# Kernel optimization log

Measured on AMD Instinct MI355X. Metric: run time of the kernel, lower is better.

## Reference

```python
import jax, jax.numpy as jnp
import numpy as np

V, DS, DF, H, NPASS = 32000, 64, 256, 8, 2
B, L, NB = 2, 1024, 512
EPS = 1e-5


def setup_inputs() -> dict:
    ks = jax.random.split(jax.random.key(0), 20)
    def n(k, shape, scale=0.02):
        return (scale * jax.random.normal(k, shape)).astype(jnp.float32)
    return {
        "token_ids": jax.random.randint(ks[0], (B, L), 0, V),
        "tok_mu": n(ks[1], (V, DS)),
        "tok_log_var": n(ks[2], (V, DS)),
        "tok_raw_alpha": n(ks[3], (V, 1), 1.0),
        "tok_features": n(ks[4], (V, DF)),
        "pos_mu": n(ks[5], (L, DS)),
        "qproj_w": n(ks[6], (H * DS, DS)),
        "qproj_b": jnp.zeros((H * DS,), jnp.float32),
        "hproj_w": n(ks[7], (DF, H * DF)),
        "hproj_b": jnp.zeros((DF,), jnp.float32),
        "mu_up_w": n(ks[8], (DS, 2 * DF)),
        "mu_up_b": jnp.zeros((DS,), jnp.float32),
        "agate_w": n(ks[9], (1, 2 * DF)),
        "agate_b": jnp.zeros((1,), jnp.float32),
        "ffn_w": n(ks[10], (DF, 2 * DF)),
        "ffn_b": jnp.zeros((DF,), jnp.float32),
        "ln_g": jnp.ones((DF,), jnp.float32),
        "ln_b": jnp.zeros((DF,), jnp.float32),
        "lm_w": n(ks[11], (V, DF)),
        "lm_b": jnp.zeros((V,), jnp.float32),
        "blob_mu": n(ks[12], (NB, DS)),
        "blob_lv": n(ks[13], (NB, DS)),
        "blob_ra": n(ks[14], (NB,), 1.0),
        "blob_f": n(ks[15], (NB, DF)),
        "bgate_w": n(ks[16], (1, 2 * DF)),
        "bgate_b": jnp.zeros((1,), jnp.float32),
    }


def _composite_weights(a):
    # front-to-back alpha compositing along last axis: w_j = a_j * prod_{k<j}(1-a_k)
    T = jnp.cumprod(1.0 - a, axis=-1)
    T_ex = jnp.concatenate([jnp.ones_like(T[..., :1]), T[..., :-1]], axis=-1)
    return a * T_ex, T[..., -1]


def _forward(token_ids, tok_mu, tok_log_var, tok_raw_alpha, tok_features, pos_mu,
             qproj_w, qproj_b, hproj_w, hproj_b, mu_up_w, mu_up_b, agate_w, agate_b,
             ffn_w, ffn_b, ln_g, ln_b, lm_w, lm_b, blob_mu, blob_lv, blob_ra, blob_f,
             bgate_w, bgate_b):
    Bc, Lc = token_ids.shape
    mu = tok_mu[token_ids] + pos_mu[:Lc][None]          # [B,L,DS]
    log_var = tok_log_var[token_ids]                     # [B,L,DS]
    alpha = jax.nn.sigmoid(tok_raw_alpha[token_ids][..., 0])  # [B,L]
    features = tok_features[token_ids]                   # [B,L,DF]

    # ---- blob query + blob render ----
    query = mu.mean(axis=1)                              # [B,DS]
    iv_b = jnp.exp(-blob_lv)                             # [NB,DS]
    d2b = (jnp.einsum('bd,nd->bn', query * query, iv_b)
           - 2.0 * jnp.einsum('bd,nd->bn', query, blob_mu * iv_b)
           + jnp.sum(blob_mu * blob_mu * iv_b, -1)[None])
    Kb = jnp.exp(-0.5 * d2b)                             # [B,NB]
    ab = jax.nn.sigmoid(blob_ra)[None] * Kb              # effective alpha
    wb, t_residual = _composite_weights(ab)
    blob_meaning = jnp.einsum('bn,nf->bf', wb, blob_f)   # [B,DF] (blob_proj = Identity)

    # ---- word meaning: multi-pass Gaussian causal render ----
    mask = jnp.tril(jnp.ones((Lc, Lc), jnp.float32))
    iv = jnp.exp(-log_var)                               # inv-variance, fixed across passes
    cur_mu, cur_alpha, cur_feat = mu, alpha, features
    meaning = None
    for p in range(NPASS):
        q = (cur_mu @ qproj_w.T + qproj_b).reshape(Bc, Lc, H, DS).transpose(0, 2, 1, 3)  # [B,H,L,DS]
        # squared Mahalanobis distance via three GEMM-style contractions (no [B,H,L,L,DS] tensor)
        d2 = (jnp.einsum('bhid,bjd->bhij', q * q, iv)
              - 2.0 * jnp.einsum('bhid,bjd->bhij', q, cur_mu * iv)
              + jnp.sum(cur_mu * cur_mu * iv, -1)[:, None, None, :])
        K = jnp.exp(-0.5 * d2)                           # [B,H,L,L]
        a = cur_alpha[:, None, None, :] * K * mask
        w, _ = _composite_weights(a)
        m = jnp.einsum('bhij,bjf->bhif', w, cur_feat)    # [B,H,L,DF]
        m_cat = m.transpose(0, 2, 1, 3).reshape(Bc, Lc, H * DF)
        meaning = m_cat @ hproj_w.T + hproj_b            # [B,L,DF] (dropout = eval/identity)
        if p < NPASS - 1:
            ctx = jnp.concatenate([cur_feat, meaning], axis=-1)  # [B,L,2DF]
            cur_mu = cur_mu + ctx @ mu_up_w.T + mu_up_b
            cur_alpha = cur_alpha * jax.nn.sigmoid(ctx @ agate_w.T + agate_b)[..., 0]
            cur_feat = cur_feat + ctx @ ffn_w.T + ffn_b

    # ---- blob gate fusion ----
    blob_exp = jnp.broadcast_to(blob_meaning[:, None, :], meaning.shape)
    gate = jax.nn.sigmoid(jnp.concatenate([blob_exp, meaning], -1) @ bgate_w.T + bgate_b)  # [B,L,1]
    t_res = t_residual[:, None, None]
    fused = (1.0 - t_res) * gate * blob_exp + t_res * meaning

    # ---- final layernorm + lm head ----
    mean = fused.mean(-1, keepdims=True)
    var = ((fused - mean) ** 2).mean(-1, keepdims=True)
    h = (fused - mean) * jax.lax.rsqrt(var + EPS) * ln_g + ln_b
    logits = h @ lm_w.T + lm_b                           # [B,L,V]
    return logits


def reference(token_ids, tok_mu, tok_log_var, tok_raw_alpha, tok_features, pos_mu,
              qproj_w, qproj_b, hproj_w, hproj_b, mu_up_w, mu_up_b, agate_w, agate_b,
              ffn_w, ffn_b, ln_g, ln_b, lm_w, lm_b, blob_mu, blob_lv, blob_ra, blob_f,
              bgate_w, bgate_b):
    return _forward(token_ids, tok_mu, tok_log_var, tok_raw_alpha, tok_features, pos_mu,
                    qproj_w, qproj_b, hproj_w, hproj_b, mu_up_w, mu_up_b, agate_w, agate_b,
                    ffn_w, ffn_b, ln_g, ln_b, lm_w, lm_b, blob_mu, blob_lv, blob_ra, blob_f,
                    bgate_w, bgate_b)
```

## Files before the change

kernel.cpp:

```cpp
#include <hip/hip_runtime.h>
#include <hip/hip_bf16.h>
#include <cstdint>
#include <cstddef>

#define V_   32000
#define DS_  64
#define DF_  256
#define H_   8
#define L_   1024
#define B_   2
#define NB_  512
#define BL_  2048
#define EPS_ 1e-5f

typedef unsigned short ushort_t;
typedef unsigned int uint_t;
typedef short bf16x8 __attribute__((ext_vector_type(8)));
typedef float f32x4 __attribute__((ext_vector_type(4)));
#define AS1 __attribute__((address_space(1)))
#define AS3 __attribute__((address_space(3)))

__device__ __forceinline__ float sigmoidf_(float x) { return 1.f / (1.f + __expf(-x)); }
__device__ __forceinline__ ushort_t f2bf(float x) {
    __hip_bfloat16 b = __float2bfloat16(x);
    return __builtin_bit_cast(ushort_t, b);
}
__device__ __forceinline__ uint_t packbf(float lo, float hi) {
    return ((uint_t)f2bf(hi) << 16) | (uint_t)f2bf(lo);
}
__device__ __forceinline__ float bflo(uint_t v) {
    return __builtin_bit_cast(float, v << 16);
}
__device__ __forceinline__ float bfhi(uint_t v) {
    return __builtin_bit_cast(float, v & 0xFFFF0000u);
}

__device__ __forceinline__ float block_reduce_sum(float v, float* red) {
    int t = threadIdx.x;
    red[t] = v;
    __syncthreads();
    for (int s = 128; s > 0; s >>= 1) {
        if (t < s) red[t] += red[t + s];
        __syncthreads();
    }
    float r = red[0];
    __syncthreads();
    return r;
}

__global__ __launch_bounds__(256) void k_cvt5(
    const float* __restrict__ s0, ushort_t* __restrict__ d0,
    const float* __restrict__ s1, ushort_t* __restrict__ d1,
    const float* __restrict__ s2, ushort_t* __restrict__ d2,
    const float* __restrict__ s3, ushort_t* __restrict__ d3,
    const float* __restrict__ s4, ushort_t* __restrict__ d4) {
    int blk = blockIdx.x;
    const float* s; ushort_t* d; int base;
    if (blk < 32)        { s = s0; d = d0; base = blk; }
    else if (blk < 64)   { s = s1; d = d1; base = blk - 32; }
    else if (blk < 192)  { s = s2; d = d2; base = blk - 64; }
    else if (blk < 704)  { s = s3; d = d3; base = blk - 192; }
    else                 { s = s4; d = d4; base = blk - 704; }
    int i = (base * 256 + threadIdx.x) * 4;
    float4 v = *reinterpret_cast<const float4*>(s + i);
    ushort4 o = {f2bf(v.x), f2bf(v.y), f2bf(v.z), f2bf(v.w)};
    *reinterpret_cast<ushort4*>(d + i) = o;
}

__global__ __launch_bounds__(256) void k_gather(
    const int* __restrict__ tok, const float* __restrict__ tok_mu,
    const float* __restrict__ tok_lv, const float* __restrict__ tok_ra,
    const float* __restrict__ tok_f, const float* __restrict__ pos_mu,
    float* __restrict__ mu, ushort_t* __restrict__ mub16,
    uint_t* __restrict__ muivP, float* __restrict__ alpha,
    float* __restrict__ feat, ushort_t* __restrict__ featb16,
    ushort_t* __restrict__ fTg) {
    int row = blockIdx.x;
    int b = row >> 10;
    int l = row & (L_ - 1);
    int t = threadIdx.x;
    int v = tok[row];
    if (t < DS_) {
        float m = tok_mu[(size_t)v * DS_ + t] + pos_mu[l * DS_ + t];
        mu[(size_t)row * DS_ + t] = m;
        mub16[(size_t)row * DS_ + t] = f2bf(m);
        float ivv = __expf(-tok_lv[(size_t)v * DS_ + t]);
        muivP[(size_t)t * BL_ + row] = packbf(m, ivv);
    }
    float fv = tok_f[(size_t)v * DF_ + t];
    feat[(size_t)row * DF_ + t] = fv;
    featb16[(size_t)row * DF_ + t] = f2bf(fv);
    {
        int jb = (l >> 3) & 7, jr = l & 7;
        int jp = (l & ~63) | ((jb ^ (t & 7)) << 3) | jr;
        fTg[((size_t)(b * DF_ + t) << 10) + jp] = f2bf(fv);
    }
    if (t == 0) alpha[row] = sigmoidf_(tok_ra[v]);
}

__global__ __launch_bounds__(256) void k_queryblob(
    const float* __restrict__ mu, const float* __restrict__ blob_mu,
    const float* __restrict__ blob_lv, const float* __restrict__ blob_ra,
    const float* __restrict__ blob_f, float* __restrict__ blobm,
    float* __restrict__ tres) {
    __shared__ float red[256];
    __shared__ float sq[DS_];
    __shared__ float sa[NB_];
    __shared__ float sp[NB_];
    int b = blockIdx.x, t = threadIdx.x;
    int d = t & 63, c = t >> 6;
    float s = 0.f;
    for (int l = c; l < L_; l += 4) s += mu[((size_t)b * L_ + l) * DS_ + d];
    red[t] = s;
    __syncthreads();
    if (c == 0)
        sq[d] = (red[d] + red[64 + d] + red[128 + d] + red[192 + d]) * (1.f / L_);
    __syncthreads();
    for (int n = t; n < NB_; n += 256) {
        float d2 = 0.f;
        for (int dd = 0; dd < DS_; ++dd) {
            float diff = sq[dd] - blob_mu[n * DS_ + dd];
            d2 += __expf(-blob_lv[n * DS_ + dd]) * diff * diff;
        }
        float a = sigmoidf_(blob_ra[n]) * __expf(-0.5f * d2);
        sa[n] = a;
        sp[n] = 1.f - a;
    }
    __syncthreads();
    int n0 = t, n1 = t + 256;
    for (int s2 = 1; s2 < NB_; s2 <<= 1) {
        float t0 = (n0 >= s2) ? sp[n0 - s2] : 1.f;
        float t1 = (n1 >= s2) ? sp[n1 - s2] : 1.f;
        __syncthreads();
        sp[n0] *= t0;
        sp[n1] *= t1;
        __syncthreads();
    }
    float w0 = sa[n0] * (n0 ? sp[n0 - 1] : 1.f);
    float w1 = sa[n1] * sp[n1 - 1];
    __syncthreads();
    sa[n0] = w0;
    sa[n1] = w1;
    if (t == 0) tres[b] = sp[NB_ - 1];
    __syncthreads();
    float acc = 0.f;
    for (int n = 0; n < NB_; ++n) acc += sa[n] * blob_f[n * DF_ + t];
    blobm[b * DF_ + t] = acc;
}

__global__ __launch_bounds__(512) void k_attn5(
    const float* __restrict__ q, const uint_t* __restrict__ muivP,
    const float* __restrict__ alpha, const ushort_t* __restrict__ fTg,
    ushort_t* __restrict__ mcatb) {
    __shared__ __align__(16) uint_t smiu[64 * 64];
    __shared__ __align__(16) ushort_t sfT[256 * 64];
    __shared__ __align__(16) ushort_t sw16[16][72];
    __shared__ float sq[H_][64];
    __shared__ float sT[H_];
    int tid = threadIdx.x;
    int w = tid >> 6, lane = tid & 63;
    int bid = blockIdx.x;
    int b = bid >> 10, i = bid & (L_ - 1);
    int row = b * L_ + i;
    const int lr = lane & 15, q4 = lane >> 4;

    for (int k = tid; k < 16 * 72; k += 512) ((ushort_t*)sw16)[k] = 0;
    sq[w][lane] = q[(size_t)row * 512 + tid];

    float T = 1.f;
    f32x4 acc0 = {}, acc1 = {};

    for (int j0 = 0; j0 <= i; j0 += 64) {
        __syncthreads();
        if (j0 > 0) {
            bool alive = false;
            #pragma unroll
            for (int h = 0; h < H_; ++h) alive |= (sT[h] >= 1e-12f);
            if (!alive) break;
        }
        {
            const uint_t* src = muivP + b * L_ + j0;
            #pragma unroll
            for (int r = 0; r < 2; ++r) {
                int d = w * 8 + r * 4 + q4;
                const uint_t* gp = src + (size_t)d * BL_ + lr * 4;
                __builtin_amdgcn_global_load_lds((const AS1 uint_t*)gp,
                    (AS3 uint_t*)&smiu[(w * 8 + r * 4) * 64], 16, 0, 0);
            }
        }
        {
            #pragma unroll
            for (int it = 0; it < 4; ++it) {
                int c0 = w * 32 + it * 8;
                const ushort_t* gp = fTg +
                    ((size_t)(b * DF_ + c0 + (lane >> 3)) << 10) + j0 + (lane & 7) * 8;
                __builtin_amdgcn_global_load_lds((const AS1 uint_t*)gp,
                    (AS3 uint_t*)&sfT[c0 * 64], 16, 0, 0);
            }
        }
        __syncthreads();

        int jj = j0 + lane;
        float d2a = 0.f;
        #pragma unroll 8
        for (int d = 0; d < 64; ++d) {
            uint_t v = smiu[d * 64 + lane];
            float m = bflo(v), iv = bfhi(v);
            float diff = sq[w][d] - m;
            d2a = fmaf(iv * diff, diff, d2a);
        }
        float a = (jj <= i) ? alpha[b * L_ + jj] * __expf(-0.5f * d2a) : 0.f;

        float p = 1.f - a;
        #pragma unroll
        for (int s = 1; s < 64; s <<= 1) {
            float tt = __shfl_up(p, s, 64);
            if (lane >= s) p *= tt;
        }
        float Tex = __shfl_up(p, 1, 64);
        if (lane == 0) Tex = 1.f;
        sw16[w][lane] = f2bf(a * T * Tex);
        float Tch = __shfl(p, 63, 64);
        T *= Tch;
        if (lane == 0) sT[w] = T;
        __syncthreads();

        #pragma unroll
        for (int kk = 0; kk < 2; ++kk) {
            bf16x8 afr = *reinterpret_cast<const bf16x8*>(
                (const char*)sw16 + lr * 144 + kk * 64 + q4 * 16);
            {
                int c = (w * 2 + 0) * 16 + lr;
                int bo = c * 128 + ((kk * 64 + q4 * 16) ^ ((c & 7) << 4));
                bf16x8 bfr = *reinterpret_cast<const bf16x8*>((const char*)sfT + bo);
                acc0 = __builtin_amdgcn_mfma_f32_16x16x32_bf16(afr, bfr, acc0, 0, 0, 0);
            }
            {
                int c = (w * 2 + 1) * 16 + lr;
                int bo = c * 128 + ((kk * 64 + q4 * 16) ^ ((c & 7) << 4));
                bf16x8 bfr = *reinterpret_cast<const bf16x8*>((const char*)sfT + bo);
                acc1 = __builtin_amdgcn_mfma_f32_16x16x32_bf16(afr, bfr, acc1, 0, 0, 0);
            }
        }
    }
    if (q4 < 2) {
        #pragma unroll
        for (int r = 0; r < 4; ++r) {
            int h = q4 * 4 + r;
            int c0 = (w * 2 + 0) * 16 + lr;
            int c1 = (w * 2 + 1) * 16 + lr;
            mcatb[(size_t)row * 2048 + h * 256 + c0] = f2bf(acc0[r]);
            mcatb[(size_t)row * 2048 + h * 256 + c1] = f2bf(acc1[r]);
        }
    }
}

template <int BM, int BN, int BK, int WGM, int WGN, bool NTS, bool WB16>
__global__ __launch_bounds__(256) void gemm_mfma2(
    const ushort_t* __restrict__ A, const ushort_t* __restrict__ A2, int K1,
    int strideA, const ushort_t* __restrict__ W, const float* __restrict__ bias,
    float* __restrict__ C, ushort_t* __restrict__ Cb, int M, int N, int K) {
    constexpr int WMF = BM / WGM / 16;
    constexpr int WNF = BN / WGN / 16;
    constexpr int KK  = BK / 32;
    constexpr int AHALF = BM * BK;
// ... 53 lines not shown
        for (int mi = 0; mi < WMF; ++mi)
            #pragma unroll
            for (int kk = 0; kk < KK; ++kk)
                af[mi][kk] = *reinterpret_cast<const bf16x8*>(
                    &Ab[((kk * 4 + q4) * BM + wr * (BM / WGM) + mi * 16 + lr) * 8]);
        #pragma unroll
        for (int ni = 0; ni < WNF; ++ni)
            #pragma unroll
            for (int kk = 0; kk < KK; ++kk)
                bfr[ni][kk] = *reinterpret_cast<const bf16x8*>(
                    &Bb[((kk * 4 + q4) * BN + wc * (BN / WGN) + ni * 16 + lr) * 8]);
        #pragma unroll
        for (int kk = 0; kk < KK; ++kk)
            #pragma unroll
            for (int mi = 0; mi < WMF; ++mi)
                #pragma unroll
                for (int ni = 0; ni < WNF; ++ni)
                    acc[mi][ni] = __builtin_amdgcn_mfma_f32_16x16x32_bf16(
                        af[mi][kk], bfr[ni][kk], acc[mi][ni], 0, 0, 0);
        __syncthreads();
    }

    float* tile = (float*)smem;
    #pragma unroll
    for (int mi = 0; mi < WMF; ++mi)
        #pragma unroll
        for (int ni = 0; ni < WNF; ++ni) {
            int col = wc * (BN / WGN) + ni * 16 + lr;
            float bv = bias[n0 + col];
            #pragma unroll
            for (int j = 0; j < 4; ++j) {
                int r2 = wr * (BM / WGM) + mi * 16 + q4 * 4 + j;
                tile[r2 * BN + col] = acc[mi][ni][j] + bv;
            }
        }
    __syncthreads();
    constexpr int EV = (BM * BN / 4) / 256;
    #pragma unroll
    for (int e = 0; e < EV; ++e) {
        int idx = e * 256 + tid;
        int r = idx / (BN / 4), c4 = idx % (BN / 4);
        f32x4 v = reinterpret_cast<const f32x4*>(tile)[idx];
        f32x4* dst = reinterpret_cast<f32x4*>(&C[(size_t)(m0 + r) * N + n0 + c4 * 4]);
        if (NTS) __builtin_nontemporal_store(v, dst);
        else *dst = v;
        if (WB16) {
            ushort4 ob = {f2bf(v[0]), f2bf(v[1]), f2bf(v[2]), f2bf(v[3])};
            *reinterpret_cast<ushort4*>(&Cb[(size_t)(m0 + r) * N + n0 + c4 * 4]) = ob;
        }
    }
}

__global__ __launch_bounds__(256) void k_apply(
    const float* __restrict__ meaning, const float* __restrict__ agw,
    const float* __restrict__ agb, const float* __restrict__ dmu,
    const float* __restrict__ dffn, float* __restrict__ mu,
    ushort_t* __restrict__ mub16, uint_t* __restrict__ muivP,
    float* __restrict__ alpha, float* __restrict__ feat,
    ushort_t* __restrict__ featb16, ushort_t* __restrict__ fTg) {
    __shared__ float red[256];
    int row = blockIdx.x, t = threadIdx.x;
    int b = row >> 10;
    int l = row & (L_ - 1);
    float c0 = feat[(size_t)row * DF_ + t];
    float c1 = meaning[(size_t)row * DF_ + t];
    float s = block_reduce_sum(c0 * agw[t] + c1 * agw[256 + t], red);
    if (t == 0) alpha[row] *= sigmoidf_(s + agb[0]);
    if (t < DS_) {
        float m = mu[(size_t)row * DS_ + t] + dmu[(size_t)row * DS_ + t];
        mu[(size_t)row * DS_ + t] = m;
        mub16[(size_t)row * DS_ + t] = f2bf(m);
        uint_t v = muivP[(size_t)t * BL_ + row];
        muivP[(size_t)t * BL_ + row] = (v & 0xFFFF0000u) | (uint_t)f2bf(m);
    }
    float fn = c0 + dffn[(size_t)row * DF_ + t];
    feat[(size_t)row * DF_ + t] = fn;
    featb16[(size_t)row * DF_ + t] = f2bf(fn);
    {
        int jb = (l >> 3) & 7, jr = l & 7;
        int jp = (l & ~63) | ((jb ^ (t & 7)) << 3) | jr;
        fTg[((size_t)(b * DF_ + t) << 10) + jp] = f2bf(fn);
    }
}

__global__ __launch_bounds__(256) void k_fused_ln(
    const float* __restrict__ meaning, const float* __restrict__ blobm,
    const float* __restrict__ tres, const float* __restrict__ bgw,
    const float* __restrict__ bgb, const float* __restrict__ ln_g,
    const float* __restrict__ ln_b, ushort_t* __restrict__ houtb) {
    __shared__ float red[256];
    int row = blockIdx.x, t = threadIdx.x;
    int b = row >> 10;
    float m = meaning[(size_t)row * DF_ + t];
    float be = blobm[b * DF_ + t];
    float tr = tres[b];
    float gsum = block_reduce_sum(be * bgw[t] + m * bgw[256 + t], red);
    float gate = sigmoidf_(gsum + bgb[0]);
    float f = (1.f - tr) * gate * be + tr * m;
    float mean = block_reduce_sum(f, red) * (1.f / DF_);
    float d = f - mean;
    float var = block_reduce_sum(d * d, red) * (1.f / DF_);
    houtb[(size_t)row * DF_ + t] = f2bf(d * rsqrtf(var + EPS_) * ln_g[t] + ln_b[t]);
}

extern "C" void kernel_launch(void* const* d_in, const int* in_sizes, int n_in,
                              void* d_out, int out_size, void* d_ws, size_t ws_size,
                              hipStream_t stream) {
    const int*   tok      = (const int*)d_in[0];
    const float* tok_mu   = (const float*)d_in[1];
    const float* tok_lv   = (const float*)d_in[2];
    const float* tok_ra   = (const float*)d_in[3];
    const float* tok_f    = (const float*)d_in[4];
    const float* pos_mu   = (const float*)d_in[5];
    const float* qproj_w  = (const float*)d_in[6];
    const float* qproj_b  = (const float*)d_in[7];
    const float* hproj_w  = (const float*)d_in[8];
    const float* hproj_b  = (const float*)d_in[9];
    const float* mu_up_w  = (const float*)d_in[10];
    const float* mu_up_b  = (const float*)d_in[11];
    const float* agate_w  = (const float*)d_in[12];
    const float* agate_b  = (const float*)d_in[13];
    const float* ffn_w    = (const float*)d_in[14];
    const float* ffn_b    = (const float*)d_in[15];
    const float* ln_g     = (const float*)d_in[16];
    const float* ln_b     = (const float*)d_in[17];
    const float* lm_w     = (const float*)d_in[18];
    const float* lm_b     = (const float*)d_in[19];
    const float* blob_mu  = (const float*)d_in[20];
    const float* blob_lv  = (const float*)d_in[21];
    const float* blob_ra  = (const float*)d_in[22];
    const float* blob_f   = (const float*)d_in[23];
    const float* bgate_w  = (const float*)d_in[24];
    const float* bgate_b  = (const float*)d_in[25];
    float* out = (float*)d_out;

    float* ws = (float*)d_ws;
    float* mu      = ws;
    float* alpha   = mu + BL_ * DS_;
    float* feat    = alpha + BL_;
    float* blobm   = feat + BL_ * DF_;
    float* tres    = blobm + B_ * DF_;
    float* q       = tres + 64;
    float* meaning = q + BL_ * 512;
    float* dmu     = meaning + BL_ * DF_;
    float* dffn    = dmu + BL_ * DS_;
    uint_t* muivP  = (uint_t*)(dffn + BL_ * DF_);
    ushort_t* fTg   = (ushort_t*)(muivP + (size_t)DS_ * BL_);
    ushort_t* mub16 = fTg + (size_t)B_ * DF_ * L_;
    ushort_t* featb16 = mub16 + (size_t)BL_ * DS_;
    ushort_t* meanb16 = featb16 + (size_t)BL_ * DF_;
    ushort_t* mcatb = meanb16 + (size_t)BL_ * DF_;
    ushort_t* hbufb = mcatb + (size_t)BL_ * 2048;
    ushort_t* wbf   = hbufb + (size_t)BL_ * DF_;
    ushort_t* hpwbf = wbf + (size_t)V_ * DF_;
    ushort_t* qpwbf = hpwbf + (size_t)DF_ * 2048;
    ushort_t* muwbf = qpwbf + (size_t)512 * 64;
    ushort_t* ffnwbf = muwbf + (size_t)64 * 512;

    k_cvt5<<<8704, 256, 0, stream>>>(qproj_w, qpwbf, mu_up_w, muwbf,
                                     ffn_w, ffnwbf, hproj_w, hpwbf, lm_w, wbf);

    k_gather<<<BL_, 256, 0, stream>>>(tok, tok_mu, tok_lv, tok_ra, tok_f, pos_mu,
                                      mu, mub16, muivP, alpha, feat, featb16, fTg);
    k_queryblob<<<B_, 256, 0, stream>>>(mu, blob_mu, blob_lv, blob_ra, blob_f,
                                        blobm, tres);

    for (int p = 0; p < 2; ++p) {
        gemm_mfma2<32, 32, 64, 2, 2, false, false>
            <<<dim3(BL_ / 32, 512 / 32), 256, 0, stream>>>(
            mub16, nullptr, 0, DS_, qpwbf, qproj_b, q, nullptr, BL_, 512, DS_);
        k_attn5<<<BL_, 512, 0, stream>>>(q, muivP, alpha, fTg, mcatb);
        if (p == 0) {
            gemm_mfma2<32, 32, 64, 2, 2, false, true>
                <<<dim3(BL_ / 32, DF_ / 32), 256, 0, stream>>>(
                mcatb, nullptr, 0, H_ * DF_, hpwbf, hproj_b, meaning, meanb16,
                BL_, DF_, H_ * DF_);
            gemm_mfma2<32, 32, 64, 2, 2, false, false>
                <<<dim3(BL_ / 32, DS_ / 32), 256, 0, stream>>>(
                featb16, meanb16, DF_, DF_, muwbf, mu_up_b, dmu, nullptr,
                BL_, DS_, 512);
            gemm_mfma2<32, 32, 64, 2, 2, false, false>
                <<<dim3(BL_ / 32, DF_ / 32), 256, 0, stream>>>(
                featb16, meanb16, DF_, DF_, ffnwbf, ffn_b, dffn, nullptr,
                BL_, DF_, 512);
            k_apply<<<BL_, 256, 0, stream>>>(meaning, agate_w, agate_b, dmu, dffn,
                                             mu, mub16, muivP, alpha, feat,
                                             featb16, fTg);
        } else {
            gemm_mfma2<32, 32, 64, 2, 2, false, false>
                <<<dim3(BL_ / 32, DF_ / 32), 256, 0, stream>>>(
                mcatb, nullptr, 0, H_ * DF_, hpwbf, hproj_b, meaning, nullptr,
                BL_, DF_, H_ * DF_);
        }
    }

    k_fused_ln<<<BL_, 256, 0, stream>>>(meaning, blobm, tres, bgate_w, bgate_b,
                                        ln_g, ln_b, hbufb);
    gemm_mfma2<128, 128, 64, 2, 2, true, false>
        <<<dim3(BL_ / 128, V_ / 128), 256, 0, stream>>>(
        hbufb, nullptr, 0, DF_, wbf, lm_b, out, nullptr, BL_, V_, DF_);
}
```

Measured before the change: 314.9 us.

## Expand Mahalanobis distance into MFMA dot products and merge setup kernels

The per-key scalar loop over 64 dims in the attention kernel is replaced by an algebraic expansion, sum(iv*q^2) - 2*sum(iv*m*q) + sum(m^2*iv). The first two terms become a 16x16x32 bf16 MFMA between per-head [q^2, -2q] rows and per-key [iv, m*iv] rows stored in a swizzled row layout. The constant term is folded into a precomputed alphaC. The conversion, gather and query-blob kernels are merged into one launch, and the blob query now recomputes mu from tokens itself. The expansion adds cancellation error in bf16, and the distance is used inside exp.

```diff
diff --git a/kernel.cpp b/kernel.cpp
--- a/kernel.cpp
+++ b/kernel.cpp
@@ -25,14 +25,8 @@
     __hip_bfloat16 b = __float2bfloat16(x);
     return __builtin_bit_cast(ushort_t, b);
 }
-__device__ __forceinline__ uint_t packbf(float lo, float hi) {
-    return ((uint_t)f2bf(hi) << 16) | (uint_t)f2bf(lo);
-}
-__device__ __forceinline__ float bflo(uint_t v) {
-    return __builtin_bit_cast(float, v << 16);
-}
-__device__ __forceinline__ float bfhi(uint_t v) {
-    return __builtin_bit_cast(float, v & 0xFFFF0000u);
+__device__ __forceinline__ float bf2f(ushort_t u) {
+    return __builtin_bit_cast(float, (uint_t)u << 16);
 }
 
 __device__ __forceinline__ float block_reduce_sum(float v, float* red) {
@@ -48,114 +42,130 @@
     return r;
 }
 
-__global__ __launch_bounds__(256) void k_cvt5(
-    const float* __restrict__ s0, ushort_t* __restrict__ d0,
-    const float* __restrict__ s1, ushort_t* __restrict__ d1,
-    const float* __restrict__ s2, ushort_t* __restrict__ d2,
-    const float* __restrict__ s3, ushort_t* __restrict__ d3,
-    const float* __restrict__ s4, ushort_t* __restrict__ d4) {
-    int blk = blockIdx.x;
-    const float* s; ushort_t* d; int base;
-    if (blk < 32)        { s = s0; d = d0; base = blk; }
-    else if (blk < 64)   { s = s1; d = d1; base = blk - 32; }
-    else if (blk < 192)  { s = s2; d = d2; base = blk - 64; }
-    else if (blk < 704)  { s = s3; d = d3; base = blk - 192; }
-    else                 { s = s4; d = d4; base = blk - 704; }
-    int i = (base * 256 + threadIdx.x) * 4;
-    float4 v = *reinterpret_cast<const float4*>(s + i);
-    ushort4 o = {f2bf(v.x), f2bf(v.y), f2bf(v.z), f2bf(v.w)};
-    *reinterpret_cast<ushort4*>(d + i) = o;
-}
-
-__global__ __launch_bounds__(256) void k_gather(
+#define NCVT_ 8704
+#define NGA_  (NCVT_ + BL_)
+#define NST_  (NGA_ + B_)
+__global__ __launch_bounds__(256) void k_setup(
     const int* __restrict__ tok, const float* __restrict__ tok_mu,
     const float* __restrict__ tok_lv, const float* __restrict__ tok_ra,
     const float* __restrict__ tok_f, const float* __restrict__ pos_mu,
+    const float* __restrict__ qproj_w, const float* __restrict__ mu_up_w,
+    const float* __restrict__ ffn_w, const float* __restrict__ hproj_w,
+    const float* __restrict__ lm_w, const float* __restrict__ blob_mu,
+    const float* __restrict__ blob_lv, const float* __restrict__ blob_ra,
+    const float* __restrict__ blob_f,
+    ushort_t* __restrict__ qpwbf, ushort_t* __restrict__ muwbf,
+    ushort_t* __restrict__ ffnwbf, ushort_t* __restrict__ hpwbf,
+    ushort_t* __restrict__ wbf,
     float* __restrict__ mu, ushort_t* __restrict__ mub16,
-    uint_t* __restrict__ muivP, float* __restrict__ alpha,
-    float* __restrict__ feat, ushort_t* __restrict__ featb16,
-    ushort_t* __restrict__ fTg) {
-    int row = blockIdx.x;
-    int b = row >> 10;
-    int l = row & (L_ - 1);
+    ushort_t* __restrict__ qkb, float* __restrict__ alpha,
+    float* __restrict__ alphaC, float* __restrict__ feat,
+    ushort_t* __restrict__ featb16, ushort_t* __restrict__ fTg,
+    float* __restrict__ blobm, float* __restrict__ tres) {
+    int blk = blockIdx.x;
     int t = threadIdx.x;
-    int v = tok[row];
-    if (t < DS_) {
-        float m = tok_mu[(size_t)v * DS_ + t] + pos_mu[l * DS_ + t];
-        mu[(size_t)row * DS_ + t] = m;
-        mub16[(size_t)row * DS_ + t] = f2bf(m);
-        float ivv = __expf(-tok_lv[(size_t)v * DS_ + t]);
-        muivP[(size_t)t * BL_ + row] = packbf(m, ivv);
-    }
-    float fv = tok_f[(size_t)v * DF_ + t];
-    feat[(size_t)row * DF_ + t] = fv;
-    featb16[(size_t)row * DF_ + t] = f2bf(fv);
-    {
+    if (blk < NCVT_) {
+        const float* s; ushort_t* d; int base;
+        if (blk < 32)        { s = qproj_w; d = qpwbf;  base = blk; }
+        else if (blk < 64)   { s = mu_up_w; d = muwbf;  base = blk - 32; }
+        else if (blk < 192)  { s = ffn_w;   d = ffnwbf; base = blk - 64; }
+        else if (blk < 704)  { s = hproj_w; d = hpwbf;  base = blk - 192; }
+        else                 { s = lm_w;    d = wbf;    base = blk - 704; }
+        int i = (base * 256 + t) * 4;
+        float4 v = *reinterpret_cast<const float4*>(s + i);
+        ushort4 o = {f2bf(v.x), f2bf(v.y), f2bf(v.z), f2bf(v.w)};
+        *reinterpret_cast<ushort4*>(d + i) = o;
+        return;
+    }
+    if (blk < NGA_) {
+        int row = blk - NCVT_;
+        int l = row & (L_ - 1);
+        int v = tok[row];
+        if (t < DS_) {
+            float m = tok_mu[(size_t)v * DS_ + t] + pos_mu[l * DS_ + t];
+            mu[(size_t)row * DS_ + t] = m;
+            mub16[(size_t)row * DS_ + t] = f2bf(m);
+            float ivv = __expf(-tok_lv[(size_t)v * DS_ + t]);
+            int sw = (row & 7) << 3;
+            qkb[(size_t)row * 128 + (t ^ sw)] = f2bf(ivv);
+            qkb[(size_t)row * 128 + 64 + (t ^ sw)] = f2bf(m * ivv);
+            float term = m * m * ivv;
+            #pragma unroll
+            for (int s2 = 1; s2 < 64; s2 <<= 1) term += __shfl_xor(term, s2, 64);
+            if (t == 0) {
+                float al = sigmoidf_(tok_ra[v]);
+                alpha[row] = al;
+                alphaC[row] = al * __expf(-0.5f * term);
+            }
+        }
+        float fv = tok_f[(size_t)v * DF_ + t];
+        feat[(size_t)row * DF_ + t] = fv;
+        featb16[(size_t)row * DF_ + t] = f2bf(fv);
         int jb = (l >> 3) & 7, jr = l & 7;
         int jp = (l & ~63) | ((jb ^ (t & 7)) << 3) | jr;
-        fTg[((size_t)(b * DF_ + t) << 10) + jp] = f2bf(fv);
-    }
-    if (t == 0) alpha[row] = sigmoidf_(tok_ra[v]);
-}
-
-__global__ __launch_bounds__(256) void k_queryblob(
-    const float* __restrict__ mu, const float* __restrict__ blob_mu,
-    const float* __restrict__ blob_lv, const float* __restrict__ blob_ra,
-    const float* __restrict__ blob_f, float* __restrict__ blobm,
-    float* __restrict__ tres) {
-    __shared__ float red[256];
-    __shared__ float sq[DS_];
-    __shared__ float sa[NB_];
-    __shared__ float sp[NB_];
-    int b = blockIdx.x, t = threadIdx.x;
-    int d = t & 63, c = t >> 6;
-    float s = 0.f;
-    for (int l = c; l < L_; l += 4) s += mu[((size_t)b * L_ + l) * DS_ + d];
-    red[t] = s;
-    __syncthreads();
-    if (c == 0)
-        sq[d] = (red[d] + red[64 + d] + red[128 + d] + red[192 + d]) * (1.f / L_);
-    __syncthreads();
-    for (int n = t; n < NB_; n += 256) {
-        float d2 = 0.f;
-        for (int dd = 0; dd < DS_; ++dd) {
-            float diff = sq[dd] - blob_mu[n * DS_ + dd];
-            d2 += __expf(-blob_lv[n * DS_ + dd]) * diff * diff;
-        }
-        float a = sigmoidf_(blob_ra[n]) * __expf(-0.5f * d2);
-        sa[n] = a;
-        sp[n] = 1.f - a;
-    }
-    __syncthreads();
-    int n0 = t, n1 = t + 256;
-    for (int s2 = 1; s2 < NB_; s2 <<= 1) {
-        float t0 = (n0 >= s2) ? sp[n0 - s2] : 1.f;
-        float t1 = (n1 >= s2) ? sp[n1 - s2] : 1.f;
-        __syncthreads();
-        sp[n0] *= t0;
-        sp[n1] *= t1;
-        __syncthreads();
-    }
-    float w0 = sa[n0] * (n0 ? sp[n0 - 1] : 1.f);
-    float w1 = sa[n1] * sp[n1 - 1];
-    __syncthreads();
-    sa[n0] = w0;
-    sa[n1] = w1;
-    if (t == 0) tres[b] = sp[NB_ - 1];
-    __syncthreads();
-    float acc = 0.f;
-    for (int n = 0; n < NB_; ++n) acc += sa[n] * blob_f[n * DF_ + t];
-    blobm[b * DF_ + t] = acc;
-}
-
-__global__ __launch_bounds__(512) void k_attn5(
-    const float* __restrict__ q, const uint_t* __restrict__ muivP,
-    const float* __restrict__ alpha, const ushort_t* __restrict__ fTg,
+        fTg[((size_t)((row >> 10) * DF_ + t) << 10) + jp] = f2bf(fv);
+        return;
+    }
+    {
+        __shared__ float red[256];
+        __shared__ int stok[L_];
+        __shared__ float sq[DS_];
+        __shared__ float sa[NB_];
+        __shared__ float sp[NB_];
+        int b = blk - NGA_;
+        for (int l = t; l < L_; l += 256) stok[l] = tok[b * L_ + l];
+        __syncthreads();
+        int d = t & 63, c = t >> 6;
+        float s = 0.f;
+        for (int l = c; l < L_; l += 4)
+            s += tok_mu[(size_t)stok[l] * DS_ + d] + pos_mu[l * DS_ + d];
+        red[t] = s;
+        __syncthreads();
+        if (c == 0)
+            sq[d] = (red[d] + red[64 + d] + red[128 + d] + red[192 + d]) * (1.f / L_);
+        __syncthreads();
+        for (int n = t; n < NB_; n += 256) {
+            float d2 = 0.f;
+            for (int dd = 0; dd < DS_; ++dd) {
+                float diff = sq[dd] - blob_mu[n * DS_ + dd];
+                d2 += __expf(-blob_lv[n * DS_ + dd]) * diff * diff;
+            }
+            float a = sigmoidf_(blob_ra[n]) * __expf(-0.5f * d2);
+            sa[n] = a;
+            sp[n] = 1.f - a;
+        }
+        __syncthreads();
+        int n0 = t, n1 = t + 256;
+        for (int s2 = 1; s2 < NB_; s2 <<= 1) {
+            float t0 = (n0 >= s2) ? sp[n0 - s2] : 1.f;
+            float t1 = (n1 >= s2) ? sp[n1 - s2] : 1.f;
+            __syncthreads();
+            sp[n0] *= t0;
+            sp[n1] *= t1;
+            __syncthreads();
+        }
+        float w0 = sa[n0] * (n0 ? sp[n0 - 1] : 1.f);
+        float w1 = sa[n1] * sp[n1 - 1];
+        __syncthreads();
+        sa[n0] = w0;
+        sa[n1] = w1;
+        if (t == 0) tres[b] = sp[NB_ - 1];
+        __syncthreads();
+        float acc = 0.f;
+        for (int n = 0; n < NB_; ++n) acc += sa[n] * blob_f[n * DF_ + t];
+        blobm[b * DF_ + t] = acc;
+    }
+}
+
+__global__ __launch_bounds__(512) void k_attn6(
+    const float* __restrict__ q, const ushort_t* __restrict__ qkb,
+    const float* __restrict__ alphaC, const ushort_t* __restrict__ fTg,
     ushort_t* __restrict__ mcatb) {
-    __shared__ __align__(16) uint_t smiu[64 * 64];
+    __shared__ __align__(16) ushort_t sQK[64 * 128];
     __shared__ __align__(16) ushort_t sfT[256 * 64];
+    __shared__ __align__(16) ushort_t sA[16 * 128];
     __shared__ __align__(16) ushort_t sw16[16][72];
-    __shared__ float sq[H_][64];
+    __shared__ float sE[H_][64];
     __shared__ float sT[H_];
     int tid = threadIdx.x;
     int w = tid >> 6, lane = tid & 63;
@@ -164,8 +174,14 @@
     int row = b * L_ + i;
     const int lr = lane & 15, q4 = lane >> 4;
 
-    for (int k = tid; k < 16 * 72; k += 512) ((ushort_t*)sw16)[k] = 0;
-    sq[w][lane] = q[(size_t)row * 512 + tid];
+    for (int k = tid; k < 8 * 128; k += 512) sA[8 * 128 + k] = 0;
+    for (int k = tid; k < 8 * 72; k += 512) ((ushort_t*)sw16)[8 * 72 + k] = 0;
+    {
+        float qv = q[(size_t)row * 512 + tid];
+        int sw = (w & 7) << 3;
+        sA[w * 128 + (lane ^ sw)] = f2bf(qv * qv);
+        sA[w * 128 + 64 + (lane ^ sw)] = f2bf(-2.f * qv);
+    }
 
     float T = 1.f;
     f32x4 acc0 = {}, acc1 = {};
@@ -179,13 +195,13 @@
             if (!alive) break;
         }
         {
-            const uint_t* src = muivP + b * L_ + j0;
-            #pragma unroll
-            for (int r = 0; r < 2; ++r) {
-                int d = w * 8 + r * 4 + q4;
-                const uint_t* gp = src + (size_t)d * BL_ + lr * 4;
-                __builtin_amdgcn_global_load_lds((const AS1 uint_t*)gp,
-                    (AS3 uint_t*)&smiu[(w * 8 + r * 4) * 64], 16, 0, 0);
+            const ushort_t* src = qkb + (size_t)(b * L_ + j0) * 128;
+            #pragma unroll
+            for (int it = 0; it < 2; ++it) {
+                int c = it * 512 + w * 64;
+                __builtin_amdgcn_global_load_lds(
+                    (const AS1 uint_t*)(src + (size_t)(c + lane) * 8),
+                    (AS3 uint_t*)&sQK[c * 8], 16, 0, 0);
             }
         }
         {
@@ -200,17 +216,28 @@
         }
         __syncthreads();
 
-        int jj = j0 + lane;
-        float d2a = 0.f;
-        #pragma unroll 8
-        for (int d = 0; d < 64; ++d) {
-            uint_t v = smiu[d * 64 + lane];
-            float m = bflo(v), iv = bfhi(v);
-            float diff = sq[w][d] - m;
-            d2a = fmaf(iv * diff, diff, d2a);
-        }
-        float a = (jj <= i) ? alpha[b * L_ + jj] * __expf(-0.5f * d2a) : 0.f;
-
+        if (w < 4) {
+            int jj = j0 + w * 16 + lr;
+            float alc = (jj <= i) ? alphaC[b * L_ + jj] : 0.f;
+            f32x4 dacc = {};
+            int j = w * 16 + lr;
+            int swj = (j & 7) << 3;
+            int swa = (lr & 7) << 3;
+            #pragma unroll
+            for (int ks = 0; ks < 4; ++ks) {
+                bf16x8 afr = *reinterpret_cast<const bf16x8*>(
+                    &sA[lr * 128 + ((ks * 32 + q4 * 8) ^ swa)]);
+                bf16x8 bfr = *reinterpret_cast<const bf16x8*>(
+                    &sQK[j * 128 + ((ks * 32 + q4 * 8) ^ swj)]);
+                dacc = __builtin_amdgcn_mfma_f32_16x16x32_bf16(afr, bfr, dacc, 0, 0, 0);
+            }
+            #pragma unroll
+            for (int r = 0; r < 4; ++r)
+                sE[q4 * 4 + r][w * 16 + lr] = alc * __expf(-0.5f * dacc[r]);
+        }
+        __syncthreads();
+
+        float a = sE[w][lane];
         float p = 1.f - a;
         #pragma unroll
         for (int s = 1; s < 64; s <<= 1) {
@@ -373,23 +400,32 @@
     const float* __restrict__ meaning, const float* __restrict__ agw,
     const float* __restrict__ agb, const float* __restrict__ dmu,
     const float* __restrict__ dffn, float* __restrict__ mu,
-    ushort_t* __restrict__ mub16, uint_t* __restrict__ muivP,
-    float* __restrict__ alpha, float* __restrict__ feat,
-    ushort_t* __restrict__ featb16, ushort_t* __restrict__ fTg) {
+    ushort_t* __restrict__ mub16, ushort_t* __restrict__ qkb,
+    float* __restrict__ alpha, float* __restrict__ alphaC,
+    float* __restrict__ feat, ushort_t* __restrict__ featb16,
+    ushort_t* __restrict__ fTg) {
     __shared__ float red[256];
     int row = blockIdx.x, t = threadIdx.x;
-    int b = row >> 10;
     int l = row & (L_ - 1);
     float c0 = feat[(size_t)row * DF_ + t];
     float c1 = meaning[(size_t)row * DF_ + t];
     float s = block_reduce_sum(c0 * agw[t] + c1 * agw[256 + t], red);
-    if (t == 0) alpha[row] *= sigmoidf_(s + agb[0]);
+    float gate = sigmoidf_(s + agb[0]);
     if (t < DS_) {
         float m = mu[(size_t)row * DS_ + t] + dmu[(size_t)row * DS_ + t];
         mu[(size_t)row * DS_ + t] = m;
         mub16[(size_t)row * DS_ + t] = f2bf(m);
-        uint_t v = muivP[(size_t)t * BL_ + row];
-        muivP[(size_t)t * BL_ + row] = (v & 0xFFFF0000u) | (uint_t)f2bf(m);
+        int sw = (row & 7) << 3;
+        float ivv = bf2f(qkb[(size_t)row * 128 + (t ^ sw)]);
+        qkb[(size_t)row * 128 + 64 + (t ^ sw)] = f2bf(m * ivv);
+        float term = m * m * ivv;
+        #pragma unroll
+        for (int s2 = 1; s2 < 64; s2 <<= 1) term += __shfl_xor(term, s2, 64);
+        if (t == 0) {
+            float aN = alpha[row] * gate;
+            alpha[row] = aN;
+            alphaC[row] = aN * __expf(-0.5f * term);
+        }
     }
     float fn = c0 + dffn[(size_t)row * DF_ + t];
     feat[(size_t)row * DF_ + t] = fn;
@@ -397,7 +433,7 @@
     {
         int jb = (l >> 3) & 7, jr = l & 7;
         int jp = (l & ~63) | ((jb ^ (t & 7)) << 3) | jr;
-        fTg[((size_t)(b * DF_ + t) << 10) + jp] = f2bf(fn);
+        fTg[((size_t)((row >> 10) * DF_ + t) << 10) + jp] = f2bf(fn);
     }
 }
 
@@ -455,15 +491,16 @@
     float* ws = (float*)d_ws;
     float* mu      = ws;
     float* alpha   = mu + BL_ * DS_;
-    float* feat    = alpha + BL_;
+    float* alphaC  = alpha + BL_;
+    float* feat    = alphaC + BL_;
     float* blobm   = feat + BL_ * DF_;
     float* tres    = blobm + B_ * DF_;
     float* q       = tres + 64;
     float* meaning = q + BL_ * 512;
     float* dmu     = meaning + BL_ * DF_;
     float* dffn    = dmu + BL_ * DS_;
-    uint_t* muivP  = (uint_t*)(dffn + BL_ * DF_);
-    ushort_t* fTg   = (ushort_t*)(muivP + (size_t)DS_ * BL_);
+    ushort_t* qkb   = (ushort_t*)(dffn + BL_ * DF_);
+    ushort_t* fTg   = qkb + (size_t)BL_ * 128;
     ushort_t* mub16 = fTg + (size_t)B_ * DF_ * L_;
     ushort_t* featb16 = mub16 + (size_t)BL_ * DS_;
     ushort_t* meanb16 = featb16 + (size_t)BL_ * DF_;
@@ -475,19 +512,18 @@
     ushort_t* muwbf = qpwbf + (size_t)512 * 64;
     ushort_t* ffnwbf = muwbf + (size_t)64 * 512;
 
-    k_cvt5<<<8704, 256, 0, stream>>>(qproj_w, qpwbf, mu_up_w, muwbf,
-                                     ffn_w, ffnwbf, hproj_w, hpwbf, lm_w, wbf);
-
-    k_gather<<<BL_, 256, 0, stream>>>(tok, tok_mu, tok_lv, tok_ra, tok_f, pos_mu,
-                                      mu, mub16, muivP, alpha, feat, featb16, fTg);
-    k_queryblob<<<B_, 256, 0, stream>>>(mu, blob_mu, blob_lv, blob_ra, blob_f,
-                                        blobm, tres);
+    k_setup<<<NST_, 256, 0, stream>>>(
+        tok, tok_mu, tok_lv, tok_ra, tok_f, pos_mu,
+        qproj_w, mu_up_w, ffn_w, hproj_w, lm_w,
+        blob_mu, blob_lv, blob_ra, blob_f,
+        qpwbf, muwbf, ffnwbf, hpwbf, wbf,
+        mu, mub16, qkb, alpha, alphaC, feat, featb16, fTg, blobm, tres);
 
     for (int p = 0; p < 2; ++p) {
         gemm_mfma2<32, 32, 64, 2, 2, false, false>
             <<<dim3(BL_ / 32, 512 / 32), 256, 0, stream>>>(
             mub16, nullptr, 0, DS_, qpwbf, qproj_b, q, nullptr, BL_, 512, DS_);
-        k_attn5<<<BL_, 512, 0, stream>>>(q, muivP, alpha, fTg, mcatb);
+        k_attn6<<<BL_, 512, 0, stream>>>(q, qkb, alphaC, fTg, mcatb);
         if (p == 0) {
             gemm_mfma2<32, 32, 64, 2, 2, false, true>
                 <<<dim3(BL_ / 32, DF_ / 32), 256, 0, stream>>>(
@@ -502,8 +538,8 @@
                 featb16, meanb16, DF_, DF_, ffnwbf, ffn_b, dffn, nullptr,
                 BL_, DF_, 512);
             k_apply<<<BL_, 256, 0, stream>>>(meaning, agate_w, agate_b, dmu, dffn,
-                                             mu, mub16, muivP, alpha, feat,
-                                             featb16, fTg);
+                                             mu, mub16, qkb, alpha, alphaC,
+                                             feat, featb16, fTg);
         } else {
             gemm_mfma2<32, 32, 64, 2, 2, false, false>
                 <<<dim3(BL_ / 32, DF_ / 32), 256, 0, stream>>>(
```

New measurement: 319.6 us. About the same (+1.5%).

## Merge setup kernels and fuse mu_up/ffn/agate GEMMs into one concatenated GEMM

Applied to the files above, without the earlier changes.

Combines the weight conversion, token gather and blob-query kernels into one launch. The blob query now recomputes the mean of mu directly from the token tables, so it no longer depends on the gather output. The mu_up, ffn and alpha-gate projections are stacked into one 352-column weight matrix, so a single GEMM replaces two GEMMs plus a block reduction in k_apply. The K tile for the h-projection and fused GEMMs also goes from 64 to 128. This cuts launch count and redundant reads, but the gate dot product is now done in bf16 and the setup kernel is less uniform.

```diff
diff --git a/kernel.cpp b/kernel.cpp
--- a/kernel.cpp
+++ b/kernel.cpp
@@ -48,104 +48,139 @@
     return r;
 }
 
-__global__ __launch_bounds__(256) void k_cvt5(
-    const float* __restrict__ s0, ushort_t* __restrict__ d0,
-    const float* __restrict__ s1, ushort_t* __restrict__ d1,
-    const float* __restrict__ s2, ushort_t* __restrict__ d2,
-    const float* __restrict__ s3, ushort_t* __restrict__ d3,
-    const float* __restrict__ s4, ushort_t* __restrict__ d4) {
-    int blk = blockIdx.x;
-    const float* s; ushort_t* d; int base;
-    if (blk < 32)        { s = s0; d = d0; base = blk; }
-    else if (blk < 64)   { s = s1; d = d1; base = blk - 32; }
-    else if (blk < 192)  { s = s2; d = d2; base = blk - 64; }
-    else if (blk < 704)  { s = s3; d = d3; base = blk - 192; }
-    else                 { s = s4; d = d4; base = blk - 704; }
-    int i = (base * 256 + threadIdx.x) * 4;
-    float4 v = *reinterpret_cast<const float4*>(s + i);
-    ushort4 o = {f2bf(v.x), f2bf(v.y), f2bf(v.z), f2bf(v.w)};
-    *reinterpret_cast<ushort4*>(d + i) = o;
-}
-
-__global__ __launch_bounds__(256) void k_gather(
+#define NCVT_ 8720
+#define NGA_  (NCVT_ + BL_)
+#define NST_  (NGA_ + B_)
+__global__ __launch_bounds__(256) void k_setup(
     const int* __restrict__ tok, const float* __restrict__ tok_mu,
     const float* __restrict__ tok_lv, const float* __restrict__ tok_ra,
     const float* __restrict__ tok_f, const float* __restrict__ pos_mu,
+    const float* __restrict__ qproj_w, const float* __restrict__ mu_up_w,
+    const float* __restrict__ mu_up_b, const float* __restrict__ ffn_w,
+    const float* __restrict__ ffn_b, const float* __restrict__ agate_w,
+    const float* __restrict__ agate_b, const float* __restrict__ hproj_w,
+    const float* __restrict__ lm_w, const float* __restrict__ blob_mu,
+    const float* __restrict__ blob_lv, const float* __restrict__ blob_ra,
+    const float* __restrict__ blob_f,
+    ushort_t* __restrict__ qpwbf, ushort_t* __restrict__ cwbf,
+    ushort_t* __restrict__ hpwbf, ushort_t* __restrict__ wbf,
+    float* __restrict__ cbias,
     float* __restrict__ mu, ushort_t* __restrict__ mub16,
     uint_t* __restrict__ muivP, float* __restrict__ alpha,
     float* __restrict__ feat, ushort_t* __restrict__ featb16,
-    ushort_t* __restrict__ fTg) {
-    int row = blockIdx.x;
-    int b = row >> 10;
-    int l = row & (L_ - 1);
+    ushort_t* __restrict__ fTg, float* __restrict__ blobm,
+    float* __restrict__ tres) {
+    int blk = blockIdx.x;
     int t = threadIdx.x;
-    int v = tok[row];
-    if (t < DS_) {
-        float m = tok_mu[(size_t)v * DS_ + t] + pos_mu[l * DS_ + t];
-        mu[(size_t)row * DS_ + t] = m;
-        mub16[(size_t)row * DS_ + t] = f2bf(m);
-        float ivv = __expf(-tok_lv[(size_t)v * DS_ + t]);
-        muivP[(size_t)t * BL_ + row] = packbf(m, ivv);
-    }
-    float fv = tok_f[(size_t)v * DF_ + t];
-    feat[(size_t)row * DF_ + t] = fv;
-    featb16[(size_t)row * DF_ + t] = f2bf(fv);
-    {
+    if (blk < 32) {
+        int i = (blk * 256 + t) * 4;
+        float4 v = *reinterpret_cast<const float4*>(qproj_w + i);
+        ushort4 o = {f2bf(v.x), f2bf(v.y), f2bf(v.z), f2bf(v.w)};
+        *reinterpret_cast<ushort4*>(qpwbf + i) = o;
+        return;
+    }
+    if (blk < 208) {
+        int i = ((blk - 32) * 256 + t) * 4;
+        int r = i >> 9, c = i & 511;
+        float4 v = {0.f, 0.f, 0.f, 0.f};
+        if (r < 64)        v = *reinterpret_cast<const float4*>(mu_up_w + r * 512 + c);
+        else if (r < 320)  v = *reinterpret_cast<const float4*>(ffn_w + (r - 64) * 512 + c);
+        else if (r == 320) v = *reinterpret_cast<const float4*>(agate_w + c);
+        ushort4 o = {f2bf(v.x), f2bf(v.y), f2bf(v.z), f2bf(v.w)};
+        *reinterpret_cast<ushort4*>(cwbf + i) = o;
+        return;
+    }
+    if (blk < 720) {
+        int i = ((blk - 208) * 256 + t) * 4;
+        float4 v = *reinterpret_cast<const float4*>(hproj_w + i);
+        ushort4 o = {f2bf(v.x), f2bf(v.y), f2bf(v.z), f2bf(v.w)};
+        *reinterpret_cast<ushort4*>(hpwbf + i) = o;
+        return;
+    }
+    if (blk < NCVT_) {
+        int i = ((blk - 720) * 256 + t) * 4;
+        float4 v = *reinterpret_cast<const float4*>(lm_w + i);
+        ushort4 o = {f2bf(v.x), f2bf(v.y), f2bf(v.z), f2bf(v.w)};
+        *reinterpret_cast<ushort4*>(wbf + i) = o;
+        return;
+    }
+    if (blk < NGA_) {
+        int row = blk - NCVT_;
+        int l = row & (L_ - 1);
+        int v = tok[row];
+        if (t < DS_) {
+            float m = tok_mu[(size_t)v * DS_ + t] + pos_mu[l * DS_ + t];
+            mu[(size_t)row * DS_ + t] = m;
+            mub16[(size_t)row * DS_ + t] = f2bf(m);
+            float ivv = __expf(-tok_lv[(size_t)v * DS_ + t]);
+            muivP[(size_t)t * BL_ + row] = packbf(m, ivv);
+        }
+        float fv = tok_f[(size_t)v * DF_ + t];
+        feat[(size_t)row * DF_ + t] = fv;
+        featb16[(size_t)row * DF_ + t] = f2bf(fv);
         int jb = (l >> 3) & 7, jr = l & 7;
         int jp = (l & ~63) | ((jb ^ (t & 7)) << 3) | jr;
-        fTg[((size_t)(b * DF_ + t) << 10) + jp] = f2bf(fv);
-    }
-    if (t == 0) alpha[row] = sigmoidf_(tok_ra[v]);
-}
-
-__global__ __launch_bounds__(256) void k_queryblob(
-    const float* __restrict__ mu, const float* __restrict__ blob_mu,
-    const float* __restrict__ blob_lv, const float* __restrict__ blob_ra,
-    const float* __restrict__ blob_f, float* __restrict__ blobm,
-    float* __restrict__ tres) {
-    __shared__ float red[256];
-    __shared__ float sq[DS_];
-    __shared__ float sa[NB_];
-    __shared__ float sp[NB_];
-    int b = blockIdx.x, t = threadIdx.x;
-    int d = t & 63, c = t >> 6;
-    float s = 0.f;
-    for (int l = c; l < L_; l += 4) s += mu[((size_t)b * L_ + l) * DS_ + d];
-    red[t] = s;
-    __syncthreads();
-    if (c == 0)
-        sq[d] = (red[d] + red[64 + d] + red[128 + d] + red[192 + d]) * (1.f / L_);
-    __syncthreads();
-    for (int n = t; n < NB_; n += 256) {
-        float d2 = 0.f;
-        for (int dd = 0; dd < DS_; ++dd) {
-            float diff = sq[dd] - blob_mu[n * DS_ + dd];
-            d2 += __expf(-blob_lv[n * DS_ + dd]) * diff * diff;
-        }
-        float a = sigmoidf_(blob_ra[n]) * __expf(-0.5f * d2);
-        sa[n] = a;
-        sp[n] = 1.f - a;
-    }
-    __syncthreads();
-    int n0 = t, n1 = t + 256;
-    for (int s2 = 1; s2 < NB_; s2 <<= 1) {
-        float t0 = (n0 >= s2) ? sp[n0 - s2] : 1.f;
-        float t1 = (n1 >= s2) ? sp[n1 - s2] : 1.f;
-        __syncthreads();
-        sp[n0] *= t0;
-        sp[n1] *= t1;
-        __syncthreads();
-    }
-    float w0 = sa[n0] * (n0 ? sp[n0 - 1] : 1.f);
-    float w1 = sa[n1] * sp[n1 - 1];
-    __syncthreads();
-    sa[n0] = w0;
-    sa[n1] = w1;
-    if (t == 0) tres[b] = sp[NB_ - 1];
-    __syncthreads();
-    float acc = 0.f;
-    for (int n = 0; n < NB_; ++n) acc += sa[n] * blob_f[n * DF_ + t];
-    blobm[b * DF_ + t] = acc;
+        fTg[((size_t)((row >> 10) * DF_ + t) << 10) + jp] = f2bf(fv);
+        if (t == 0) alpha[row] = sigmoidf_(tok_ra[v]);
+        return;
+    }
+    if (blk < NST_) {
+        __shared__ float red[256];
+        __shared__ int stok[L_];
+        __shared__ float sq[DS_];
+        __shared__ float sa[NB_];
+        __shared__ float sp[NB_];
+        int b = blk - NGA_;
+        for (int l = t; l < L_; l += 256) stok[l] = tok[b * L_ + l];
+        __syncthreads();
+        int d = t & 63, c = t >> 6;
+        float s = 0.f;
+        for (int l = c; l < L_; l += 4)
+            s += tok_mu[(size_t)stok[l] * DS_ + d] + pos_mu[l * DS_ + d];
+        red[t] = s;
+        __syncthreads();
+        if (c == 0)
+            sq[d] = (red[d] + red[64 + d] + red[128 + d] + red[192 + d]) * (1.f / L_);
+        __syncthreads();
+        for (int n = t; n < NB_; n += 256) {
+            float d2 = 0.f;
+            for (int dd = 0; dd < DS_; ++dd) {
+                float diff = sq[dd] - blob_mu[n * DS_ + dd];
+                d2 += __expf(-blob_lv[n * DS_ + dd]) * diff * diff;
+            }
+            float a = sigmoidf_(blob_ra[n]) * __expf(-0.5f * d2);
+            sa[n] = a;
+            sp[n] = 1.f - a;
+        }
+        __syncthreads();
+        int n0 = t, n1 = t + 256;
+        for (int s2 = 1; s2 < NB_; s2 <<= 1) {
+            float t0 = (n0 >= s2) ? sp[n0 - s2] : 1.f;
+            float t1 = (n1 >= s2) ? sp[n1 - s2] : 1.f;
+            __syncthreads();
+            sp[n0] *= t0;
+            sp[n1] *= t1;
+            __syncthreads();
+        }
+        float w0 = sa[n0] * (n0 ? sp[n0 - 1] : 1.f);
+        float w1 = sa[n1] * sp[n1 - 1];
+        __syncthreads();
+        sa[n0] = w0;
+        sa[n1] = w1;
+        if (t == 0) tres[b] = sp[NB_ - 1];
+        __syncthreads();
+        float acc = 0.f;
+        for (int n = 0; n < NB_; ++n) acc += sa[n] * blob_f[n * DF_ + t];
+        blobm[b * DF_ + t] = acc;
+        return;
+    }
+    for (int idx = t; idx < 352; idx += 256) {
+        float bv = 0.f;
+        if (idx < 64) bv = mu_up_b[idx];
+        else if (idx < 320) bv = ffn_b[idx - 64];
+        else if (idx == 320) bv = agate_b[0];
+        cbias[idx] = bv;
+    }
 }
 
 __global__ __launch_bounds__(512) void k_attn5(
@@ -370,35 +405,27 @@
 }
 
 __global__ __launch_bounds__(256) void k_apply(
-    const float* __restrict__ meaning, const float* __restrict__ agw,
-    const float* __restrict__ agb, const float* __restrict__ dmu,
-    const float* __restrict__ dffn, float* __restrict__ mu,
+    const float* __restrict__ dctx, float* __restrict__ mu,
     ushort_t* __restrict__ mub16, uint_t* __restrict__ muivP,
     float* __restrict__ alpha, float* __restrict__ feat,
     ushort_t* __restrict__ featb16, ushort_t* __restrict__ fTg) {
-    __shared__ float red[256];
     int row = blockIdx.x, t = threadIdx.x;
-    int b = row >> 10;
     int l = row & (L_ - 1);
-    float c0 = feat[(size_t)row * DF_ + t];
-    float c1 = meaning[(size_t)row * DF_ + t];
-    float s = block_reduce_sum(c0 * agw[t] + c1 * agw[256 + t], red);
-    if (t == 0) alpha[row] *= sigmoidf_(s + agb[0]);
+    const float* dr = dctx + (size_t)row * 352;
+    if (t == 0) alpha[row] *= sigmoidf_(dr[320]);
     if (t < DS_) {
-        float m = mu[(size_t)row * DS_ + t] + dmu[(size_t)row * DS_ + t];
+        float m = mu[(size_t)row * DS_ + t] + dr[t];
         mu[(size_t)row * DS_ + t] = m;
         mub16[(size_t)row * DS_ + t] = f2bf(m);
         uint_t v = muivP[(size_t)t * BL_ + row];
         muivP[(size_t)t * BL_ + row] = (v & 0xFFFF0000u) | (uint_t)f2bf(m);
     }
-    float fn = c0 + dffn[(size_t)row * DF_ + t];
+    float fn = feat[(size_t)row * DF_ + t] + dr[64 + t];
     feat[(size_t)row * DF_ + t] = fn;
     featb16[(size_t)row * DF_ + t] = f2bf(fn);
-    {
-        int jb = (l >> 3) & 7, jr = l & 7;
-        int jp = (l & ~63) | ((jb ^ (t & 7)) << 3) | jr;
-        fTg[((size_t)(b * DF_ + t) << 10) + jp] = f2bf(fn);
-    }
+    int jb = (l >> 3) & 7, jr = l & 7;
+    int jp = (l & ~63) | ((jb ^ (t & 7)) << 3) | jr;
+    fTg[((size_t)((row >> 10) * DF_ + t) << 10) + jp] = f2bf(fn);
 }
 
 __global__ __launch_bounds__(256) void k_fused_ln(
@@ -460,9 +487,9 @@
     float* tres    = blobm + B_ * DF_;
     float* q       = tres + 64;
     float* meaning = q + BL_ * 512;
-    float* dmu     = meaning + BL_ * DF_;
-    float* dffn    = dmu + BL_ * DS_;
-    uint_t* muivP  = (uint_t*)(dffn + BL_ * DF_);
+    float* dctx    = meaning + BL_ * DF_;
+    float* cbias   = dctx + (size_t)BL_ * 352;
+    uint_t* muivP  = (uint_t*)(cbias + 384);
     ushort_t* fTg   = (ushort_t*)(muivP + (size_t)DS_ * BL_);
     ushort_t* mub16 = fTg + (size_t)B_ * DF_ * L_;
     ushort_t* featb16 = mub16 + (size_t)BL_ * DS_;
@@ -472,16 +499,14 @@
     ushort_t* wbf   = hbufb + (size_t)BL_ * DF_;
     ushort_t* hpwbf = wbf + (size_t)V_ * DF_;
     ushort_t* qpwbf = hpwbf + (size_t)DF_ * 2048;
-    ushort_t* muwbf = qpwbf + (size_t)512 * 64;
-    ushort_t* ffnwbf = muwbf + (size_t)64 * 512;
-
-    k_cvt5<<<8704, 256, 0, stream>>>(qproj_w, qpwbf, mu_up_w, muwbf,
-                                     ffn_w, ffnwbf, hproj_w, hpwbf, lm_w, wbf);
-
-    k_gather<<<BL_, 256, 0, stream>>>(tok, tok_mu, tok_lv, tok_ra, tok_f, pos_mu,
-                                      mu, mub16, muivP, alpha, feat, featb16, fTg);
-    k_queryblob<<<B_, 256, 0, stream>>>(mu, blob_mu, blob_lv, blob_ra, blob_f,
-                                        blobm, tres);
+    ushort_t* cwbf  = qpwbf + (size_t)512 * 64;
+
+    k_setup<<<NST_ + 1, 256, 0, stream>>>(
+        tok, tok_mu, tok_lv, tok_ra, tok_f, pos_mu,
+        qproj_w, mu_up_w, mu_up_b, ffn_w, ffn_b, agate_w, agate_b,
+        hproj_w, lm_w, blob_mu, blob_lv, blob_ra, blob_f,
+        qpwbf, cwbf, hpwbf, wbf, cbias,
+        mu, mub16, muivP, alpha, feat, featb16, fTg, blobm, tres);
 
     for (int p = 0; p < 2; ++p) {
         gemm_mfma2<32, 32, 64, 2, 2, false, false>
@@ -489,23 +514,18 @@
             mub16, nullptr, 0, DS_, qpwbf, qproj_b, q, nullptr, BL_, 512, DS_);
         k_attn5<<<BL_, 512, 0, stream>>>(q, muivP, alpha, fTg, mcatb);
         if (p == 0) {
-            gemm_mfma2<32, 32, 64, 2, 2, false, true>
+            gemm_mfma2<32, 32, 128, 2, 2, false, true>
                 <<<dim3(BL_ / 32, DF_ / 32), 256, 0, stream>>>(
                 mcatb, nullptr, 0, H_ * DF_, hpwbf, hproj_b, meaning, meanb16,
                 BL_, DF_, H_ * DF_);
-            gemm_mfma2<32, 32, 64, 2, 2, false, false>
-                <<<dim3(BL_ / 32, DS_ / 32), 256, 0, stream>>>(
-                featb16, meanb16, DF_, DF_, muwbf, mu_up_b, dmu, nullptr,
-                BL_, DS_, 512);
-            gemm_mfma2<32, 32, 64, 2, 2, false, false>
-                <<<dim3(BL_ / 32, DF_ / 32), 256, 0, stream>>>(
-                featb16, meanb16, DF_, DF_, ffnwbf, ffn_b, dffn, nullptr,
-                BL_, DF_, 512);
-            k_apply<<<BL_, 256, 0, stream>>>(meaning, agate_w, agate_b, dmu, dffn,
-                                             mu, mub16, muivP, alpha, feat,
-                                             featb16, fTg);
+            gemm_mfma2<32, 32, 128, 2, 2, false, false>
+                <<<dim3(BL_ / 32, 352 / 32), 256, 0, stream>>>(
+                featb16, meanb16, DF_, DF_, cwbf, cbias, dctx, nullptr,
+                BL_, 352, 512);
+            k_apply<<<BL_, 256, 0, stream>>>(dctx, mu, mub16, muivP, alpha,
+                                             feat, featb16, fTg);
         } else {
-            gemm_mfma2<32, 32, 64, 2, 2, false, false>
+            gemm_mfma2<32, 32, 128, 2, 2, false, false>
                 <<<dim3(BL_ / 32, DF_ / 32), 256, 0, stream>>>(
                 mcatb, nullptr, 0, H_ * DF_, hpwbf, hproj_b, meaning, nullptr,
                 BL_, DF_, H_ * DF_);
```

Measured after the change: 312.0 us. No clear change (-0.9%).
